# Optimization experiments

Measured on AMD Instinct MI355X. Metric: run time of the kernel, lower is better.

The kernel has to match this reference:

```python
import jax, jax.numpy as jnp
import numpy as np

NUM_HEADS = 16
HEAD_DIM = 64  # latent_dim // num_heads = 1024 // 16


def setup_inputs() -> dict:
    key = jax.random.key(0)
    k1, k2, k3, k4 = jax.random.split(key, 4)
    B, S, C = 4, 2048, 1024
    x = jax.random.normal(k1, (B, S, C), dtype=jnp.float32)
    # torch nn.Linear weight layout: [out_features, in_features]
    W_qkv = jax.random.normal(k2, (2 * 1024 + C, C), dtype=jnp.float32) * (C ** -0.5)
    W_out = jax.random.normal(k3, (C, C), dtype=jnp.float32) * (C ** -0.5)
    b_out = jax.random.normal(k4, (C,), dtype=jnp.float32) * 0.01
    return {"x": x, "W_qkv": W_qkv, "W_out": W_out, "b_out": b_out}


def reference(x, W_qkv, W_out, b_out):
    B, S, C = x.shape
    H, CH = NUM_HEADS, HEAD_DIM
    qkv = jnp.einsum('bsc,oc->bso', x, W_qkv)          # [B, S, 2*latent + C]
    qkv = qkv.reshape(B, S, H, -1)                      # per-head: [CH, CH, C//H]
    q = qkv[..., :CH]
    k = qkv[..., CH:2 * CH]
    v = qkv[..., 2 * CH:]
    energy = jnp.einsum('bqhc,bkhc->bhqk', q, k)        # full score matrix
    scale = jnp.asarray(C, x.dtype) ** 0.5              # note: original scales by sqrt(C), not sqrt(head_dim)
    attn = jax.nn.softmax(energy / scale, axis=-1)
    out = jnp.einsum('bhqk,bkhc->bqhc', attn, v).reshape(B, S, -1)
    out = jnp.einsum('bsc,oc->bso', out, W_out) + b_out
    return out + x
```

## Files before the change

kernel.cpp:

```cpp
#include <hip/hip_runtime.h>
#include <hip/hip_bf16.h>
#include <stdint.h>

#define BB 4
#define SS 2048
#define CC 1024
#define HH 16
#define DD 64
#define MTOT (BB*SS)
#define NQKV 3072

typedef __attribute__((ext_vector_type(8))) short short8;
typedef __attribute__((ext_vector_type(4))) float f32x4;

#define MFMA16(A,B,C) __builtin_amdgcn_mfma_f32_16x16x32_bf16((A),(B),(C),0,0,0)
#define BARRIER() asm volatile("s_barrier" ::: "memory")

__device__ __forceinline__ ushort f2bf(float f) {
  uint32_t u = __builtin_bit_cast(uint32_t, f);
  u += 0x7FFFu + ((u >> 16) & 1u);
  return (ushort)(u >> 16);
}

__device__ __forceinline__ unsigned cvtpk(float lo, float hi) {
  unsigned r;
  asm("v_cvt_pk_bf16_f32 %0, %1, %2" : "=v"(r) : "v"(lo), "v"(hi));
  return r;
}

__device__ __forceinline__ float hw_exp2(float x) {
  float r;
  asm("v_exp_f32 %0, %1" : "=v"(r) : "v"(x));
  return r;
}

__global__ void cvt3_kernel(const float* __restrict__ a, ushort* __restrict__ da, int na4,
                            const float* __restrict__ b, ushort* __restrict__ db, int nb4,
                            const float* __restrict__ c, ushort* __restrict__ dc, int nc4) {
  int total = na4 + nb4 + nc4;
  int stride = gridDim.x * blockDim.x;
  for (int i = blockIdx.x * blockDim.x + threadIdx.x; i < total; i += stride) {
    const float4* s; ushort4* d; int k;
    if (i < na4)            { s = (const float4*)a; d = (ushort4*)da; k = i; }
    else if (i < na4 + nb4) { s = (const float4*)b; d = (ushort4*)db; k = i - na4; }
    else                    { s = (const float4*)c; d = (ushort4*)dc; k = i - na4 - nb4; }
    float4 v = s[k];
    ushort4 o;
    o.x = f2bf(v.x); o.y = f2bf(v.y); o.z = f2bf(v.z); o.w = f2bf(v.w);
    d[k] = o;
  }
}

__device__ __forceinline__ void stage_half128(const ushort* __restrict__ gsrc, ushort* ldsbase, int tid) {
  #pragma unroll
  for (int ld = 0; ld < 4; ++ld) {
    int ci = ld * 256 + tid;
    int row = ci >> 3, slot = ci & 7;
    const ushort* src = gsrc + (size_t)row * 1024 + ((slot ^ (row & 7)) << 3);
    __builtin_amdgcn_global_load_lds(
        (const __attribute__((address_space(1))) uint32_t*)src,
        (__attribute__((address_space(3))) uint32_t*)(ldsbase + ci * 8), 16, 0, 0);
  }
}

__device__ __forceinline__ short8 rd_frag(const ushort* Lb, int row, int slot) {
  return *(const short8*)(Lb + row * 64 + ((slot ^ (row & 7)) << 3));
}

__device__ __forceinline__ void core128(const ushort* __restrict__ A, const ushort* __restrict__ Bw,
                                        int m0, int n0, ushort* L, f32x4 acc[4][4]) {
  const int tid = threadIdx.x, lane = tid & 63, w = tid >> 6;
  const int q = lane & 15, g = lane >> 4;
  const int wm = (w >> 1) * 64, wn = (w & 1) * 64;
  const ushort* Ag = A + (size_t)m0 * 1024;
  const ushort* Bg = Bw + (size_t)n0 * 1024;

  #pragma unroll
  for (int tt = 0; tt < 2; ++tt) {
    stage_half128(Ag + tt * 64, L + tt * 16384, tid);
    stage_half128(Bg + tt * 64, L + tt * 16384 + 8192, tid);
  }
  asm volatile("s_waitcnt vmcnt(8)" ::: "memory");
  BARRIER();

  #pragma unroll 1
  for (int t = 0; t < 16; ++t) {
    const ushort* La = L + (t & 1) * 16384;
    const ushort* Lb = La + 8192;
    short8 af[4][2], bf[4][2];
    #pragma unroll
    for (int mi = 0; mi < 4; ++mi)
      #pragma unroll
      for (int ks = 0; ks < 2; ++ks)
        af[mi][ks] = rd_frag(La, wm + mi * 16 + q, ks * 4 + g);
    #pragma unroll
    for (int nj = 0; nj < 4; ++nj)
      #pragma unroll
      for (int ks = 0; ks < 2; ++ks)
        bf[nj][ks] = rd_frag(Lb, wn + nj * 16 + q, ks * 4 + g);
    #pragma unroll
    for (int mi = 0; mi < 4; ++mi)
      #pragma unroll
      for (int nj = 0; nj < 4; ++nj) {
        acc[mi][nj] = MFMA16(af[mi][0], bf[nj][0], acc[mi][nj]);
        acc[mi][nj] = MFMA16(af[mi][1], bf[nj][1], acc[mi][nj]);
      }
    BARRIER();
    if (t <= 13) {
      ushort* Ls = L + (t & 1) * 16384;
      stage_half128(Ag + (t + 2) * 64, Ls, tid);
      stage_half128(Bg + (t + 2) * 64, Ls + 8192, tid);
      asm volatile("s_waitcnt vmcnt(8)" ::: "memory");
      BARRIER();
    } else if (t == 14) {
      asm volatile("s_waitcnt vmcnt(0)" ::: "memory");
      BARRIER();
    }
  }
}

__global__ __launch_bounds__(256, 2) void gemm_qkv(const ushort* __restrict__ xb, const ushort* __restrict__ wqkv,
                                                   ushort* __restrict__ qfbuf, ushort* __restrict__ kfbuf,
                                                   ushort* __restrict__ vfbuf) {
  __shared__ __align__(16) ushort L[32768];
  const int bid = blockIdx.x;
  const int xcd = bid & 7, r0 = bid >> 3;
  const int m0 = (r0 / 3) * 128, n0 = (xcd * 3 + (r0 % 3)) * 128;

  f32x4 acc[4][4];
  #pragma unroll
  for (int i = 0; i < 4; ++i)
    #pragma unroll
    for (int j = 0; j < 4; ++j) acc[i][j] = f32x4{0.f, 0.f, 0.f, 0.f};
  core128(xb, wqkv, m0, n0, L, acc);

  const int lane = threadIdx.x & 63, wave = threadIdx.x >> 6;
  const int g = lane >> 4, q = lane & 15;
  const int wm = (wave >> 1) * 64, wn = (wave & 1) * 64;
  const int s0 = m0 & 2047, bb = m0 >> 11;

  #pragma unroll
  for (int j = 0; j < 4; ++j) {
    int n = n0 + wn + j * 16 + q;
    int h = n / 192;
    int which = (n - h * 192) >> 6;
    float scl = (which == 0) ? 0.045084222f : 1.0f;
    int nc = wn + j * 16 + q;
    #pragma unroll
    for (int i = 0; i < 4; ++i) {
      #pragma unroll
      for (int rr = 0; rr < 4; ++rr) {
        int mr = wm + i * 16 + g * 4 + rr;
        L[mr * 128 + (nc ^ ((mr & 7) << 4))] = f2bf(acc[i][j][rr] * scl);
      }
    }
  }
  __syncthreads();

  {
    const int n_g = n0 + wave * 32;
    const int h = n_g / 192, rem = n_g - h * 192, which = rem >> 6;
    const int bh = bb * 16 + h;
    if (which < 2) {
      ushort* dst0 = (which == 0) ? qfbuf : kfbuf;
      const int c0 = (rem & 63) >> 5;
      #pragma unroll
      for (int k = 0; k < 8; ++k) {
        int jt = (s0 >> 4) + k;
        int mr = k * 16 + (lane & 15);
        int nc0 = wave * 32 + (lane >> 4) * 8;
        short8 v = *(const short8*)(L + mr * 128 + (nc0 ^ ((mr & 7) << 4)));
        *(short8*)(dst0 + ((((size_t)bh * 128 + jt) * 2 + c0) * 64 + lane) * 8) = v;
      }
    } else {
      const int ct0 = (rem & 63) >> 4;
      #pragma unroll
      for (int k = 0; k < 8; ++k) {
        int jcr = k >> 1, ct = ct0 + (k & 1);
        int nc = wave * 32 + (k & 1) * 16 + (lane & 15);
        int mrb = jcr * 32 + (lane >> 4) * 8;
        short8 v;
        #pragma unroll
        for (int e = 0; e < 8; ++e) {
          int mr = mrb + e;
          v[e] = (short)L[mr * 128 + (nc ^ ((mr & 7) << 4))];
        }
        int jc = (s0 >> 5) + jcr;
        *(short8*)(vfbuf + ((((size_t)bh * 64 + jc) * 4 + ct) * 64 + lane) * 8) = v;
      }
    }
  }
}

__global__ __launch_bounds__(256, 2) void gemm_out(const ushort* __restrict__ ab, const ushort* __restrict__ wout,
                                                   const float* __restrict__ x, const float* __restrict__ bias,
                                                   float* __restrict__ out) {
  __shared__ __align__(16) ushort L[32768];
  const int bid = blockIdx.x;
  const int sw = (bid & 7) * 64 + (bid >> 3);
  const int m0 = (sw & 63) * 128, n0 = (sw >> 6) * 128;

  f32x4 acc[4][4];
  #pragma unroll
  for (int i = 0; i < 4; ++i)
    #pragma unroll
    for (int j = 0; j < 4; ++j) acc[i][j] = f32x4{0.f, 0.f, 0.f, 0.f};
  core128(ab, wout, m0, n0, L, acc);

  const int lane = threadIdx.x & 63, wave = threadIdx.x >> 6;
  const int g = lane >> 4, q = lane & 15;
  const int wm = (wave >> 1) * 64, wn = (wave & 1) * 64;
  #pragma unroll
  for (int j = 0; j < 4; ++j) {
    int n = n0 + wn + j * 16 + q;
    float bj = bias[n];
    #pragma unroll
    for (int i = 0; i < 4; ++i) {
      int mb = m0 + wm + i * 16 + g * 4;
      #pragma unroll
      for (int rr = 0; rr < 4; ++rr) {
        size_t m = (size_t)(mb + rr);
        out[m * CC + n] = acc[i][j][rr] + bj + x[m * CC + n];
      }
    }
  }
}

__device__ __forceinline__ void attn_step(const short8 kf[4][2], const short8 vf[2][4],
                                          const short8 qf[2][2], const short8 onesf,
                                          f32x4 oa[2][4], f32x4 la[2],
                                          ushort* pw0, int g, int q) {
  const f32x4 zed = {0.f, 0.f, 0.f, 0.f};
  #pragma unroll
  for (int t = 0; t < 2; ++t) {
    f32x4 sa[4];
    __builtin_amdgcn_s_setprio(1);
    #pragma unroll
    for (int jt = 0; jt < 4; ++jt) {
      sa[jt] = MFMA16(kf[jt][0], qf[t][0], zed);
      sa[jt] = MFMA16(kf[jt][1], qf[t][1], sa[jt]);
    }
    __builtin_amdgcn_s_setprio(0);
    ushort* pw = pw0 + t * 1152;
    #pragma unroll
    for (int jt = 0; jt < 4; ++jt) {
      uint2 wv;
      wv.x = cvtpk(hw_exp2(sa[jt][0]), hw_exp2(sa[jt][1]));
      wv.y = cvtpk(hw_exp2(sa[jt][2]), hw_exp2(sa[jt][3]));
      *reinterpret_cast<uint2*>(pw + q * 72 + jt * 16 + 4 * g) = wv;
    }
    #pragma unroll
    for (int jc = 0; jc < 2; ++jc) {
      short8 pa = *reinterpret_cast<const short8*>(pw + q * 72 + jc * 32 + g * 8);
      __builtin_amdgcn_s_setprio(1);
      #pragma unroll
      for (int ct = 0; ct < 4; ++ct)
        oa[t][ct] = MFMA16(pa, vf[jc][ct], oa[t][ct]);
      la[t] = MFMA16(pa, onesf, la[t]);
      __builtin_amdgcn_s_setprio(0);
    }
  }
}

__global__ __launch_bounds__(256) void attn_kernel(const ushort* __restrict__ QF, const ushort* __restrict__ KF,
                                                   const ushort* __restrict__ VF, ushort* __restrict__ aout) {
  __shared__ ushort Ps[4][2][16 * 72];
  const int bid = blockIdx.x;
  const int xcd = bid & 7, rr = bid >> 3;
  const int qb = rr & 15, bh = xcd + (rr >> 4) * 8;
  const int lane = threadIdx.x & 63, wave = threadIdx.x >> 6;
  const int g = lane >> 4, q = lane & 15;
  const int qt0 = (qb * 4 + wave) * 2;
  const f32x4 zed = {0.f, 0.f, 0.f, 0.f};

  const ushort* Qb = QF + (size_t)bh * 131072 + lane * 8;
  const ushort* Kp = KF + (size_t)bh * 131072 + lane * 8;
  const ushort* Vp = VF + (size_t)bh * 131072 + lane * 8;
  ushort* pw0 = Ps[wave][0];

  short8 onesf;
  #pragma unroll
  for (int e = 0; e < 8; ++e) onesf[e] = (short)0x3F80;

  short8 qf[2][2];
  #pragma unroll
  for (int t = 0; t < 2; ++t)
    #pragma unroll
    for (int c0 = 0; c0 < 2; ++c0)
      qf[t][c0] = *(const short8*)(Qb + ((size_t)(qt0 + t) * 2 + c0) * 512);

  f32x4 oa[2][4], la[2];
  #pragma unroll
  for (int t = 0; t < 2; ++t) {
    la[t] = zed;
    #pragma unroll
    for (int ct = 0; ct < 4; ++ct) oa[t][ct] = zed;
  }

  short8 kfA[4][2], kfB[4][2], vfA[2][4], vfB[2][4];
  #pragma unroll
  for (int jt = 0; jt < 4; ++jt)
    #pragma unroll
    for (int c0 = 0; c0 < 2; ++c0)
      kfA[jt][c0] = *(const short8*)(Kp + ((size_t)jt * 2 + c0) * 512);

  #pragma unroll 1
  for (int i = 0; i < 32; i += 2) {
    #pragma unroll
    for (int jc = 0; jc < 2; ++jc)
      #pragma unroll
      for (int ct = 0; ct < 4; ++ct)
        vfA[jc][ct] = *(const short8*)(Vp + ((size_t)jc * 4 + ct) * 512);
    #pragma unroll
    for (int jt = 0; jt < 4; ++jt)
      #pragma unroll
      for (int c0 = 0; c0 < 2; ++c0)
        kfB[jt][c0] = *(const short8*)(Kp + 4096 + ((size_t)jt * 2 + c0) * 512);

    attn_step(kfA, vfA, qf, onesf, oa, la, pw0, g, q);

    #pragma unroll
    for (int jc = 0; jc < 2; ++jc)
      #pragma unroll
      for (int ct = 0; ct < 4; ++ct)
        vfB[jc][ct] = *(const short8*)(Vp + 4096 + ((size_t)jc * 4 + ct) * 512);
    if (i + 2 < 32) {
      #pragma unroll
      for (int jt = 0; jt < 4; ++jt)
        #pragma unroll
        for (int c0 = 0; c0 < 2; ++c0)
          kfA[jt][c0] = *(const short8*)(Kp + 8192 + ((size_t)jt * 2 + c0) * 512);
    }

    attn_step(kfB, vfB, qf, onesf, oa, la, pw0, g, q);

    Kp += 8192; Vp += 8192;
  }

  const int b = bh >> 4, h = bh & 15;
  #pragma unroll
  for (int t = 0; t < 2; ++t) {
    float inv[4];
    #pragma unroll
    for (int r2 = 0; r2 < 4; ++r2) inv[r2] = 1.0f / la[t][r2];
    #pragma unroll
    for (int ct = 0; ct < 4; ++ct) {
      size_t rowb = (size_t)b * SS + (qt0 + t) * 16 + 4 * g;
      int col = h * DD + ct * 16 + q;
      aout[(rowb + 0) * CC + col] = f2bf(oa[t][ct][0] * inv[0]);
      aout[(rowb + 1) * CC + col] = f2bf(oa[t][ct][1] * inv[1]);
      aout[(rowb + 2) * CC + col] = f2bf(oa[t][ct][2] * inv[2]);
      aout[(rowb + 3) * CC + col] = f2bf(oa[t][ct][3] * inv[3]);
    }
  }
}

extern "C" void kernel_launch(void* const* d_in, const int* in_sizes, int n_in,
                              void* d_out, int out_size, void* d_ws, size_t ws_size,
                              hipStream_t stream) {
  const float* x    = (const float*)d_in[0];
  const float* wqkv = (const float*)d_in[1];
  const float* wout = (const float*)d_in[2];
  const float* bias = (const float*)d_in[3];
  float* out = (float*)d_out;

  ushort* xb    = (ushort*)d_ws;
  ushort* wqkvb = xb + (size_t)8 * 1024 * 1024;
  ushort* woutb = wqkvb + (size_t)3 * 1024 * 1024;
  ushort* qfbuf = woutb + (size_t)1024 * 1024;
  ushort* kfbuf = qfbuf + (size_t)8 * 1024 * 1024;
  ushort* vfbuf = kfbuf + (size_t)8 * 1024 * 1024;
  ushort* aout  = vfbuf + (size_t)8 * 1024 * 1024;

  hipLaunchKernelGGL(cvt3_kernel, dim3(2048), dim3(256), 0, stream,
                     x, xb, 8 * 1024 * 1024 / 4,
                     wqkv, wqkvb, 3 * 1024 * 1024 / 4,
                     wout, woutb, 1024 * 1024 / 4);

  hipLaunchKernelGGL(gemm_qkv, dim3(1536), dim3(256), 0, stream,
                     xb, wqkvb, qfbuf, kfbuf, vfbuf);
  hipLaunchKernelGGL(attn_kernel, dim3(1024), dim3(256), 0, stream,
                     qfbuf, kfbuf, vfbuf, aout);
  hipLaunchKernelGGL(gemm_out, dim3(512), dim3(256), 0, stream,
                     aout, woutb, x, bias, out);
}
```

Before: 191.2 us.

## Software-pipeline attention QK and PV steps, stage gemm_out epilogue through LDS

The attention loop now splits each step into a QK/exp pack phase and a PV accumulate phase. The PV of the previous K block is interleaved after the QK of the next one, using double-buffered P tiles in LDS, and the kernel asks for three blocks per CU. The gemm_out epilogue writes the accumulators to swizzled LDS and then does coalesced float4 reads of bias and residual and float4 stores. It also reads the residual from the bf16 copy of x instead of fp32 x, which halves that traffic but adds bf16 rounding error to the residual term.

```diff
diff --git a/kernel.cpp b/kernel.cpp
--- a/kernel.cpp
+++ b/kernel.cpp
@@ -20,6 +20,10 @@
   uint32_t u = __builtin_bit_cast(uint32_t, f);
   u += 0x7FFFu + ((u >> 16) & 1u);
   return (ushort)(u >> 16);
+}
+
+__device__ __forceinline__ float bf2f(ushort u) {
+  return __builtin_bit_cast(float, (uint32_t)u << 16);
 }
 
 __device__ __forceinline__ unsigned cvtpk(float lo, float hi) {
@@ -193,7 +197,7 @@
 }
 
 __global__ __launch_bounds__(256, 2) void gemm_out(const ushort* __restrict__ ab, const ushort* __restrict__ wout,
-                                                   const float* __restrict__ x, const float* __restrict__ bias,
+                                                   const ushort* __restrict__ xbb, const float* __restrict__ bias,
                                                    float* __restrict__ out) {
   __shared__ __align__(16) ushort L[32768];
   const int bid = blockIdx.x;
@@ -207,29 +211,48 @@
     for (int j = 0; j < 4; ++j) acc[i][j] = f32x4{0.f, 0.f, 0.f, 0.f};
   core128(ab, wout, m0, n0, L, acc);
 
-  const int lane = threadIdx.x & 63, wave = threadIdx.x >> 6;
+  const int tid = threadIdx.x;
+  const int lane = tid & 63, wave = tid >> 6;
   const int g = lane >> 4, q = lane & 15;
   const int wm = (wave >> 1) * 64, wn = (wave & 1) * 64;
+  float* Lf = reinterpret_cast<float*>(L);
+
   #pragma unroll
   for (int j = 0; j < 4; ++j) {
-    int n = n0 + wn + j * 16 + q;
-    float bj = bias[n];
+    int nc = wn + j * 16 + q;
     #pragma unroll
     for (int i = 0; i < 4; ++i) {
-      int mb = m0 + wm + i * 16 + g * 4;
       #pragma unroll
       for (int rr = 0; rr < 4; ++rr) {
-        size_t m = (size_t)(mb + rr);
-        out[m * CC + n] = acc[i][j][rr] + bj + x[m * CC + n];
+        int mr = wm + i * 16 + g * 4 + rr;
+        int swz = ((mr & 4) << 0) | ((mr & 8) << 1);
+        Lf[mr * 128 + (nc ^ swz)] = acc[i][j][rr];
       }
     }
   }
-}
-
-__device__ __forceinline__ void attn_step(const short8 kf[4][2], const short8 vf[2][4],
-                                          const short8 qf[2][2], const short8 onesf,
-                                          f32x4 oa[2][4], f32x4 la[2],
-                                          ushort* pw0, int g, int q) {
+  __syncthreads();
+
+  #pragma unroll
+  for (int k = 0; k < 16; ++k) {
+    int ci = k * 256 + tid;
+    int row = ci >> 5, cb = (ci & 31) * 4;
+    int swz = ((row & 4) << 0) | ((row & 8) << 1);
+    float4 v = *(const float4*)(Lf + row * 128 + (cb ^ swz));
+    size_t m = (size_t)(m0 + row);
+    int n = n0 + cb;
+    ushort4 xr = *(const ushort4*)(xbb + m * 1024 + n);
+    float4 bv = *(const float4*)(bias + n);
+    float4 o;
+    o.x = v.x + bv.x + bf2f(xr.x);
+    o.y = v.y + bv.y + bf2f(xr.y);
+    o.z = v.z + bv.z + bf2f(xr.z);
+    o.w = v.w + bv.w + bf2f(xr.w);
+    *(float4*)(out + m * 1024 + n) = o;
+  }
+}
+
+__device__ __forceinline__ void qk_pack(const short8 kf[4][2], const short8 qf[2][2],
+                                        ushort* pwPar, int g, int q) {
   const f32x4 zed = {0.f, 0.f, 0.f, 0.f};
   #pragma unroll
   for (int t = 0; t < 2; ++t) {
@@ -241,7 +264,7 @@
       sa[jt] = MFMA16(kf[jt][1], qf[t][1], sa[jt]);
     }
     __builtin_amdgcn_s_setprio(0);
-    ushort* pw = pw0 + t * 1152;
+    ushort* pw = pwPar + t * 1152;
     #pragma unroll
     for (int jt = 0; jt < 4; ++jt) {
       uint2 wv;
@@ -249,6 +272,15 @@
       wv.y = cvtpk(hw_exp2(sa[jt][2]), hw_exp2(sa[jt][3]));
       *reinterpret_cast<uint2*>(pw + q * 72 + jt * 16 + 4 * g) = wv;
     }
+  }
+}
+
+__device__ __forceinline__ void pv_acc(const short8 vf[2][4], const ushort* pwPar,
+                                       const short8 onesf, f32x4 oa[2][4], f32x4 la[2],
+                                       int g, int q) {
+  #pragma unroll
+  for (int t = 0; t < 2; ++t) {
+    const ushort* pw = pwPar + t * 1152;
     #pragma unroll
     for (int jc = 0; jc < 2; ++jc) {
       short8 pa = *reinterpret_cast<const short8*>(pw + q * 72 + jc * 32 + g * 8);
@@ -262,9 +294,9 @@
   }
 }
 
-__global__ __launch_bounds__(256) void attn_kernel(const ushort* __restrict__ QF, const ushort* __restrict__ KF,
-                                                   const ushort* __restrict__ VF, ushort* __restrict__ aout) {
-  __shared__ ushort Ps[4][2][16 * 72];
+__global__ __launch_bounds__(256, 3) void attn_kernel(const ushort* __restrict__ QF, const ushort* __restrict__ KF,
+                                                      const ushort* __restrict__ VF, ushort* __restrict__ aout) {
+  __shared__ ushort Ps[4][2][2 * 1152];
   const int bid = blockIdx.x;
   const int xcd = bid & 7, rr = bid >> 3;
   const int qb = rr & 15, bh = xcd + (rr >> 4) * 8;
@@ -276,7 +308,6 @@
   const ushort* Qb = QF + (size_t)bh * 131072 + lane * 8;
   const ushort* Kp = KF + (size_t)bh * 131072 + lane * 8;
   const ushort* Vp = VF + (size_t)bh * 131072 + lane * 8;
-  ushort* pw0 = Ps[wave][0];
 
   short8 onesf;
   #pragma unroll
@@ -305,7 +336,7 @@
       kfA[jt][c0] = *(const short8*)(Kp + ((size_t)jt * 2 + c0) * 512);
 
   #pragma unroll 1
-  for (int i = 0; i < 32; i += 2) {
+  for (int ii = 0; ii < 32; ii += 2) {
     #pragma unroll
     for (int jc = 0; jc < 2; ++jc)
       #pragma unroll
@@ -317,14 +348,15 @@
       for (int c0 = 0; c0 < 2; ++c0)
         kfB[jt][c0] = *(const short8*)(Kp + 4096 + ((size_t)jt * 2 + c0) * 512);
 
-    attn_step(kfA, vfA, qf, onesf, oa, la, pw0, g, q);
+    qk_pack(kfA, qf, Ps[wave][0], g, q);
+    if (ii > 0) pv_acc(vfB, Ps[wave][1], onesf, oa, la, g, q);
 
     #pragma unroll
     for (int jc = 0; jc < 2; ++jc)
       #pragma unroll
       for (int ct = 0; ct < 4; ++ct)
         vfB[jc][ct] = *(const short8*)(Vp + 4096 + ((size_t)jc * 4 + ct) * 512);
-    if (i + 2 < 32) {
+    if (ii + 2 < 32) {
       #pragma unroll
       for (int jt = 0; jt < 4; ++jt)
         #pragma unroll
@@ -332,10 +364,12 @@
           kfA[jt][c0] = *(const short8*)(Kp + 8192 + ((size_t)jt * 2 + c0) * 512);
     }
 
-    attn_step(kfB, vfB, qf, onesf, oa, la, pw0, g, q);
+    qk_pack(kfB, qf, Ps[wave][1], g, q);
+    pv_acc(vfA, Ps[wave][0], onesf, oa, la, g, q);
 
     Kp += 8192; Vp += 8192;
   }
+  pv_acc(vfB, Ps[wave][1], onesf, oa, la, g, q);
 
   const int b = bh >> 4, h = bh & 15;
   #pragma unroll
@@ -382,5 +416,5 @@
   hipLaunchKernelGGL(attn_kernel, dim3(1024), dim3(256), 0, stream,
                      qfbuf, kfbuf, vfbuf, aout);
   hipLaunchKernelGGL(gemm_out, dim3(512), dim3(256), 0, stream,
-                     aout, woutb, x, bias, out);
-}
+                     aout, woutb, xb, bias, out);
+}
```

Result: slower. 502.1 us (+162.6%).
